# Kernel tuning notes

Measured on AMD Instinct MI355X. Metric: run time of the kernel, lower is better.

The kernel has to match this reference:

```python
import jax, jax.numpy as jnp
import numpy as np

N_NODES = 100000
N_EDGES = 3200000
F_IN = 128
HIDDEN = 16
F_OUT = 2


def setup_inputs() -> dict:
    key = jax.random.key(0)
    k1, k2, k3, k4 = jax.random.split(key, 4)
    x = jax.random.normal(k1, (N_NODES, F_IN), dtype=jnp.float32)
    edge_index = jax.random.randint(k2, (2, N_EDGES), 0, N_NODES, dtype=jnp.int64)
    # Glorot-ish init like torch_geometric's GCNConv linear layers
    W1 = jax.random.normal(k3, (F_IN, HIDDEN), dtype=jnp.float32) * (1.0 / np.sqrt(F_IN))
    b1 = jnp.zeros((HIDDEN,), dtype=jnp.float32)
    W2 = jax.random.normal(k4, (HIDDEN, F_OUT), dtype=jnp.float32) * (1.0 / np.sqrt(HIDDEN))
    b2 = jnp.zeros((F_OUT,), dtype=jnp.float32)
    return {"x": x, "edge_index": edge_index, "W1": W1, "b1": b1, "W2": W2, "b2": b2}


def _gcn_conv(x, src, dst, W, b, num_nodes):
    """PyG GCNConv: out = D^{-1/2}(A+I)D^{-1/2} X W + b (self-loops included in src/dst)."""
    h = x @ W  # [N, F_out]
    ones = jnp.ones(src.shape[0], dtype=h.dtype)
    deg = jax.ops.segment_sum(ones, dst, num_segments=num_nodes)  # in-degree incl. self-loop
    deg_inv_sqrt = jnp.where(deg > 0, jax.lax.rsqrt(jnp.maximum(deg, 1.0)), 0.0)
    norm = deg_inv_sqrt[src] * deg_inv_sqrt[dst]  # [E+N]
    msg = h[src] * norm[:, None]  # gather + scale: [E+N, F_out]
    out = jax.ops.segment_sum(msg, dst, num_segments=num_nodes)  # scatter-add
    return out + b


def reference(x, edge_index, W1, b1, W2, b2):
    num_nodes = x.shape[0]
    self_loops = jnp.arange(num_nodes, dtype=edge_index.dtype)
    src = jnp.concatenate([edge_index[0], self_loops])
    dst = jnp.concatenate([edge_index[1], self_loops])
    h = jax.nn.relu(_gcn_conv(x, src, dst, W1, b1, num_nodes))
    # F.dropout(training=self.training) is identity in eval mode
    out = _gcn_conv(h, src, dst, W2, b2, num_nodes)
    return out
```

## Files before the change

kernel.cpp:

```cpp
#include <hip/hip_runtime.h>

#define N_NODES 100000
#define N_EDGES 3200000
#define F_IN    128
#define HIDDEN  16
#define F_OUT   2

#define BSZ     256
#define NB      391
#define NPAD    (NB * BSZ)
#define G       800
#define EPB     (N_EDGES / G)
#define DUMMY_E 100000u

typedef float  f32x4 __attribute__((ext_vector_type(4)));
typedef float  f32x2 __attribute__((ext_vector_type(2)));
typedef _Float16 half8 __attribute__((ext_vector_type(8)));
typedef _Float16 half4 __attribute__((ext_vector_type(4)));

__global__ __launch_bounds__(256) void k_hist(const int* __restrict__ dst,
                                              unsigned* __restrict__ blockHist) {
    __shared__ unsigned h0[NB];
    __shared__ unsigned h1[NB];
    int t = threadIdx.x, g = blockIdx.x;
    for (int i = t; i < NB; i += 256) { h0[i] = 0u; h1[i] = 0u; }
    __syncthreads();
    const int2* d2 = (const int2*)(dst + g * EPB);
    unsigned* myh = (t & 1) ? h1 : h0;
    for (int i = t; i < EPB / 2; i += 256) {
        int2 v = d2[i];
        atomicAdd(&myh[(unsigned)v.x >> 8], 1u);
        atomicAdd(&myh[(unsigned)v.y >> 8], 1u);
    }
    __syncthreads();
    for (int i = t; i < NB; i += 256) blockHist[i * G + g] = h0[i] + h1[i];
}

__global__ __launch_bounds__(1024) void k_scan_blocks(unsigned* __restrict__ blockHist,
                                                      unsigned* __restrict__ total) {
    __shared__ unsigned s[1024];
    int b = blockIdx.x, t = threadIdx.x;
    unsigned v = (t < G) ? blockHist[b * G + t] : 0u;
    s[t] = v;
    __syncthreads();
    for (int off = 1; off < 1024; off <<= 1) {
        unsigned xv = (t >= off) ? s[t - off] : 0u;
        __syncthreads();
        s[t] += xv;
        __syncthreads();
    }
    if (t < G) blockHist[b * G + t] = s[t] - v;
    if (t == 1023) total[b] = s[t];
}

__global__ __launch_bounds__(512) void k_scan_buckets(const unsigned* __restrict__ total,
                                                      unsigned* __restrict__ bucketBase,
                                                      int* __restrict__ rowstart) {
    __shared__ unsigned s[512];
    int t = threadIdx.x;
    unsigned v = (t < NB) ? total[t] : 0u;
    s[t] = v;
    __syncthreads();
    for (int off = 1; off < 512; off <<= 1) {
        unsigned xv = (t >= off) ? s[t - off] : 0u;
        __syncthreads();
        s[t] += xv;
        __syncthreads();
    }
    if (t < NB) bucketBase[t] = s[t] - v;
    if (t == 511) {
        bucketBase[NB] = s[t];
        rowstart[N_NODES] = (int)s[t];
    }
}

__global__ __launch_bounds__(256) void k_scatter(const int* __restrict__ src,
                                                 const int* __restrict__ dst,
                                                 const unsigned* __restrict__ blockHist,
                                                 const unsigned* __restrict__ bucketBase,
                                                 unsigned* __restrict__ adj) {
    __shared__ unsigned stage[EPB];
    __shared__ unsigned short stage_b[EPB];
    __shared__ unsigned hist[NB];
    __shared__ unsigned h1[NB];
    __shared__ unsigned lstart[NB];
    __shared__ unsigned gbase[NB];
    __shared__ unsigned ssum[256];
    int t = threadIdx.x, g = blockIdx.x;
    for (int i = t; i < NB; i += 256) {
        hist[i] = 0u; h1[i] = 0u;
        gbase[i] = bucketBase[i] + blockHist[i * G + g];
    }
    __syncthreads();
    const int2* s2 = (const int2*)(src + g * EPB);
    const int2* d2 = (const int2*)(dst + g * EPB);
    unsigned* myh = (t & 1) ? h1 : hist;
    for (int i = t; i < EPB / 2; i += 256) {
        int2 v = d2[i];
        atomicAdd(&myh[(unsigned)v.x >> 8], 1u);
        atomicAdd(&myh[(unsigned)v.y >> 8], 1u);
    }
    __syncthreads();
    int i0 = t * 2;
    unsigned v0 = (i0 + 0 < NB) ? hist[i0 + 0] + h1[i0 + 0] : 0u;
    unsigned v1 = (i0 + 1 < NB) ? hist[i0 + 1] + h1[i0 + 1] : 0u;
    unsigned my = v0 + v1;
    ssum[t] = my;
    __syncthreads();
    for (int off = 1; off < 256; off <<= 1) {
        unsigned xv = (t >= off) ? ssum[t - off] : 0u;
        __syncthreads();
        ssum[t] += xv;
        __syncthreads();
    }
    unsigned e0 = ssum[t] - my;
    __syncthreads();
    unsigned e1 = e0 + v0;
    if (i0 + 0 < NB) { lstart[i0 + 0] = e0; hist[i0 + 0] = e0; }
    if (i0 + 1 < NB) { lstart[i0 + 1] = e1; hist[i0 + 1] = e1; }
    __syncthreads();
    for (int i = t; i < EPB / 2; i += 256) {
        int2 sv = s2[i], dv = d2[i];
        unsigned bkt0 = (unsigned)dv.x >> 8;
        unsigned pos0 = atomicAdd(&hist[bkt0], 1u);
        stage[pos0] = ((unsigned)(dv.x & 255) << 17) | (unsigned)sv.x;
        stage_b[pos0] = (unsigned short)bkt0;
        unsigned bkt1 = (unsigned)dv.y >> 8;
        unsigned pos1 = atomicAdd(&hist[bkt1], 1u);
        stage[pos1] = ((unsigned)(dv.y & 255) << 17) | (unsigned)sv.y;
        stage_b[pos1] = (unsigned short)bkt1;
    }
    __syncthreads();
    for (int j = t; j < EPB; j += 256) {
        unsigned bkt = stage_b[j];
        adj[gbase[bkt] + (j - lstart[bkt])] = stage[j];
    }
}

__global__ __launch_bounds__(512) void k_sortbucket(const unsigned* __restrict__ adj,
                                                    const unsigned* __restrict__ bucketBase,
                                                    unsigned* __restrict__ adj2,
                                                    int* __restrict__ rowstart,
                                                    float* __restrict__ dinv) {
    __shared__ unsigned hist[BSZ];
    __shared__ unsigned sc[BSZ];
    __shared__ unsigned cur[BSZ];
    int b = blockIdx.x, t = threadIdx.x;
    if (t < BSZ) hist[t] = 0u;
    __syncthreads();
    int e0 = (int)bucketBase[b], e1 = (int)bucketBase[b + 1];
    for (int i = e0 + t; i < e1; i += 512) atomicAdd(&hist[adj[i] >> 17], 1u);
    __syncthreads();
    if (t < BSZ) sc[t] = hist[t];
    __syncthreads();
    for (int off = 1; off < BSZ; off <<= 1) {
        unsigned a = 0;
        if (t < BSZ && t >= off) a = sc[t - off];
        __syncthreads();
        if (t < BSZ) sc[t] += a;
        __syncthreads();
    }
    if (t < BSZ) {
        unsigned excl = sc[t] - hist[t];
        cur[t] = (unsigned)e0 + excl;
        int node = b * BSZ + t;
        if (node < N_NODES) {
            rowstart[node] = e0 + (int)excl;
            dinv[node] = rsqrtf((float)(hist[t] + 1u));
        }
    }
    __syncthreads();
    for (int i = e0 + t; i < e1; i += 512) {
        unsigned v = adj[i];
        unsigned pos = atomicAdd(&cur[v >> 17], 1u);
        adj2[pos] = v & 0x1FFFFu;
    }
}

#define MM1_NODES 64
#define SXP 132
__global__ __launch_bounds__(256) void k_mm1(const float* __restrict__ x,
                                             const float* __restrict__ W1,
                                             const float* __restrict__ dinv,
                                             half4* __restrict__ hs) {
    __shared__ float sW[F_IN * HIDDEN];
    __shared__ float sX[MM1_NODES * SXP];
    int t = threadIdx.x;
    for (int i = t; i < F_IN * HIDDEN; i += 256) sW[i] = W1[i];
    int node0 = blockIdx.x * MM1_NODES;
    const float4* xv = (const float4*)(x + (size_t)node0 * F_IN);
    int maxv = (N_NODES - node0) * (F_IN / 4);
    if (maxv < 0) maxv = 0;
    for (int i = t; i < MM1_NODES * (F_IN / 4); i += 256) {
        if (i < maxv) {
            int nl = i >> 5, f4 = i & 31;
            ((float4*)(sX + nl * SXP))[f4] = xv[i];
        }
    }
    __syncthreads();
    int lane4 = t & 3;
    int nl = t >> 2;
    int n = node0 + nl;
    if (n >= NPAD) return;
    if (n >= N_NODES) {
        half4 hz = {(_Float16)0.f, (_Float16)0.f, (_Float16)0.f, (_Float16)0.f};
        hs[(size_t)n * 4 + lane4] = hz;
        return;
    }
    const float4* sWv = (const float4*)sW;
    float4 a = {0.f, 0.f, 0.f, 0.f};
    #pragma unroll 8
    for (int f = 0; f < F_IN; ++f) {
        float xval = sX[nl * SXP + f];
        float4 w = sWv[f * 4 + lane4];
        a.x = fmaf(xval, w.x, a.x);
        a.y = fmaf(xval, w.y, a.y);
        a.z = fmaf(xval, w.z, a.z);
        a.w = fmaf(xval, w.w, a.w);
    }
    float dv = dinv[n];
    half4 h; h[0] = (_Float16)(a.x * dv); h[1] = (_Float16)(a.y * dv);
    h[2] = (_Float16)(a.z * dv); h[3] = (_Float16)(a.w * dv);
    hs[(size_t)n * 4 + lane4] = h;
}

__global__ __launch_bounds__(256) void k_agg1(const unsigned* __restrict__ adj2,
                                              const int* __restrict__ rowstart,
                                              const char* __restrict__ hs,
                                              const float* __restrict__ dinv,
                                              const float* __restrict__ b1,
                                              const float* __restrict__ W2,
                                              float2* __restrict__ hs2) {
    int g = blockIdx.x * 256 + threadIdx.x;
    int node = g >> 1, le = g & 1;
    if (node >= N_NODES) {
        if (le == 0 && node < NPAD) { float2 z = {0.f, 0.f}; hs2[node] = z; }
        return;
    }
    int rs = rowstart[node], re = rowstart[node + 1];
    unsigned le16 = (unsigned)le * 16u;
    unsigned dummy_off = DUMMY_E * 32u + le16;

    float a0 = 0.f, a1 = 0.f, a2 = 0.f, a3 = 0.f, a4 = 0.f, a5 = 0.f, a6 = 0.f, a7 = 0.f;
    f32x4 w0, w1, w2, w3, w4, w5, w6, w7;

#define GL1(dst, o) asm volatile("global_load_dwordx4 %0, %1, %2" \
    : "=v"(dst) : "v"(o), "s"(hs) : "memory");
#define AC1(w_) { half8 h8; __builtin_memcpy(&h8, &w_, 16); \
    a0 += (float)h8[0]; a1 += (float)h8[1]; a2 += (float)h8[2]; a3 += (float)h8[3]; \
    a4 += (float)h8[4]; a5 += (float)h8[5]; a6 += (float)h8[6]; a7 += (float)h8[7]; }

    for (int bs = rs; bs < re; bs += 8) {
        const unsigned* ap = adj2 + bs;
        unsigned j0 = ap[0], j1 = ap[1], j2 = ap[2], j3 = ap[3];
        unsigned j4 = ap[4], j5 = ap[5], j6 = ap[6], j7 = ap[7];
        unsigned o0 = (bs + 0 < re) ? (j0 << 5) + le16 : dummy_off;
        unsigned o1 = (bs + 1 < re) ? (j1 << 5) + le16 : dummy_off;
        unsigned o2 = (bs + 2 < re) ? (j2 << 5) + le16 : dummy_off;
        unsigned o3 = (bs + 3 < re) ? (j3 << 5) + le16 : dummy_off;
        unsigned o4 = (bs + 4 < re) ? (j4 << 5) + le16 : dummy_off;
        unsigned o5 = (bs + 5 < re) ? (j5 << 5) + le16 : dummy_off;
        unsigned o6 = (bs + 6 < re) ? (j6 << 5) + le16 : dummy_off;
        unsigned o7 = (bs + 7 < re) ? (j7 << 5) + le16 : dummy_off;
        GL1(w0, o0) GL1(w1, o1) GL1(w2, o2) GL1(w3, o3)
        GL1(w4, o4) GL1(w5, o5) GL1(w6, o6) GL1(w7, o7)
        asm volatile("s_waitcnt vmcnt(0)" ::: "memory");
        __builtin_amdgcn_sched_barrier(0);
        AC1(w0) AC1(w1) AC1(w2) AC1(w3) AC1(w4) AC1(w5) AC1(w6) AC1(w7)
    }
    const _Float16* selfrow = (const _Float16*)(hs + (size_t)node * 32 + le16);
    float dv = dinv[node];
    float q0 = dv * (a0 + (float)selfrow[0]), q1 = dv * (a1 + (float)selfrow[1]);
    float q2 = dv * (a2 + (float)selfrow[2]), q3 = dv * (a3 + (float)selfrow[3]);
    float q4 = dv * (a4 + (float)selfrow[4]), q5 = dv * (a5 + (float)selfrow[5]);
    float q6 = dv * (a6 + (float)selfrow[6]), q7 = dv * (a7 + (float)selfrow[7]);
    const float4* b1v = (const float4*)(b1 + le * 8);
    float4 ba = b1v[0], bb = b1v[1];
    const float4* w2v = (const float4*)(W2 + le * 16);
    float4 wA = w2v[0], wB = w2v[1], wC = w2v[2], wD = w2v[3];
    float p0 = 0.f, p1 = 0.f, r;
    r = fmaxf(q0 + ba.x, 0.f); p0 = fmaf(r, wA.x, p0); p1 = fmaf(r, wA.y, p1);
    r = fmaxf(q1 + ba.y, 0.f); p0 = fmaf(r, wA.z, p0); p1 = fmaf(r, wA.w, p1);
    r = fmaxf(q2 + ba.z, 0.f); p0 = fmaf(r, wB.x, p0); p1 = fmaf(r, wB.y, p1);
    r = fmaxf(q3 + ba.w, 0.f); p0 = fmaf(r, wB.z, p0); p1 = fmaf(r, wB.w, p1);
    r = fmaxf(q4 + bb.x, 0.f); p0 = fmaf(r, wC.x, p0); p1 = fmaf(r, wC.y, p1);
    r = fmaxf(q5 + bb.y, 0.f); p0 = fmaf(r, wC.z, p0); p1 = fmaf(r, wC.w, p1);
    r = fmaxf(q6 + bb.z, 0.f); p0 = fmaf(r, wD.x, p0); p1 = fmaf(r, wD.y, p1);
    r = fmaxf(q7 + bb.w, 0.f); p0 = fmaf(r, wD.z, p0); p1 = fmaf(r, wD.w, p1);
    p0 += __shfl_xor(p0, 1);
    p1 += __shfl_xor(p1, 1);
    if (le == 0) {
        float2 h2; h2.x = p0 * dv; h2.y = p1 * dv;
        hs2[node] = h2;
    }
}

__global__ __launch_bounds__(256) void k_agg2(const unsigned* __restrict__ adj2,
                                              const int* __restrict__ rowstart,
                                              const char* __restrict__ hs2,
                                              const float* __restrict__ dinv,
                                              const float* __restrict__ b2,
                                              float2* __restrict__ out) {
    int node = blockIdx.x * 256 + threadIdx.x;
    if (node >= N_NODES) return;
    int rs = rowstart[node], re = rowstart[node + 1];
    unsigned dummy_off = DUMMY_E * 8u;

    float a0 = 0.f, a1 = 0.f;
    f32x2 w0, w1, w2, w3, w4, w5, w6, w7;

#define GL2(dst, o) asm volatile("global_load_dwordx2 %0, %1, %2" \
    : "=v"(dst) : "v"(o), "s"(hs2) : "memory");

    for (int bs = rs; bs < re; bs += 8) {
        const unsigned* ap = adj2 + bs;
        unsigned j0 = ap[0], j1 = ap[1], j2 = ap[2], j3 = ap[3];
        unsigned j4 = ap[4], j5 = ap[5], j6 = ap[6], j7 = ap[7];
        unsigned o0 = (bs + 0 < re) ? (j0 << 3) : dummy_off;
        unsigned o1 = (bs + 1 < re) ? (j1 << 3) : dummy_off;
        unsigned o2 = (bs + 2 < re) ? (j2 << 3) : dummy_off;
        unsigned o3 = (bs + 3 < re) ? (j3 << 3) : dummy_off;
        unsigned o4 = (bs + 4 < re) ? (j4 << 3) : dummy_off;
        unsigned o5 = (bs + 5 < re) ? (j5 << 3) : dummy_off;
        unsigned o6 = (bs + 6 < re) ? (j6 << 3) : dummy_off;
        unsigned o7 = (bs + 7 < re) ? (j7 << 3) : dummy_off;
        GL2(w0, o0) GL2(w1, o1) GL2(w2, o2) GL2(w3, o3)
        GL2(w4, o4) GL2(w5, o5) GL2(w6, o6) GL2(w7, o7)
        asm volatile("s_waitcnt vmcnt(0)" ::: "memory");
        __builtin_amdgcn_sched_barrier(0);
        a0 += w0[0] + w1[0] + w2[0] + w3[0] + w4[0] + w5[0] + w6[0] + w7[0];
        a1 += w0[1] + w1[1] + w2[1] + w3[1] + w4[1] + w5[1] + w6[1] + w7[1];
    }
    const float2* h2p = (const float2*)hs2;
    float2 selfv = h2p[node];
    float dv = dinv[node];
    float2 r;
    r.x = fmaf(dv, a0 + selfv.x, b2[0]);
    r.y = fmaf(dv, a1 + selfv.y, b2[1]);
    out[node] = r;
}

extern "C" void kernel_launch(void* const* d_in, const int* in_sizes, int n_in,
                              void* d_out, int out_size, void* d_ws, size_t ws_size,
                              hipStream_t stream) {
    const float* x   = (const float*)d_in[0];
    const int*   ei  = (const int*)d_in[1];
    const int*   srcv = ei;
    const int*   dstv = ei + N_EDGES;
    const float* W1  = (const float*)d_in[2];
    const float* b1  = (const float*)d_in[3];
    const float* W2  = (const float*)d_in[4];
    const float* b2  = (const float*)d_in[5];
    float* out = (float*)d_out;

    char* w = (char*)d_ws;
    unsigned* adj        = (unsigned*)w;  w += (size_t)N_EDGES * 4;
    unsigned* adj2       = (unsigned*)w;  w += (size_t)(N_EDGES + 8) * 4;
    unsigned* blockHist  = (unsigned*)w;  w += (size_t)NB * G * 4;
    unsigned* total      = (unsigned*)w;  w += (size_t)NB * 4;
    unsigned* bucketBase = (unsigned*)w;  w += (size_t)(NB + 1) * 4;
    int*      rowstart   = (int*)w;       w += (size_t)(N_NODES + 1) * 4;
    w = (char*)(((size_t)w + 15) & ~(size_t)15);
    float* dinv  = (float*)w;  w += (size_t)N_NODES * 4;
    char*  hs    = w;          w += (size_t)NPAD * HIDDEN * 2;
    float* hs2   = (float*)w;

    k_hist        <<<G, 256, 0, stream>>>(dstv, blockHist);
    k_scan_blocks <<<NB, 1024, 0, stream>>>(blockHist, total);
    k_scan_buckets<<<1, 512, 0, stream>>>(total, bucketBase, rowstart);
    k_scatter     <<<G, 256, 0, stream>>>(srcv, dstv, blockHist, bucketBase, adj);
    k_sortbucket  <<<NB, 512, 0, stream>>>(adj, bucketBase, adj2, rowstart, dinv);
    k_mm1         <<<NPAD / MM1_NODES, 256, 0, stream>>>(x, W1, dinv, (half4*)hs);
    k_agg1        <<<(2 * NPAD) / 256, 256, 0, stream>>>(adj2, rowstart, hs, dinv,
                                                         b1, W2, (float2*)hs2);
    k_agg2        <<<(NPAD + 255) / 256, 256, 0, stream>>>(adj2, rowstart, (const char*)hs2,
                                                           dinv, b2, (float2*)out);
}
```

Measured before the change: 125.0 us.

## Fuse bucket scan into block scan and fold first matmul into bucket sort

Merges the two scan kernels using a last-block ticket counter, so the final bucket-level scan runs in whichever block finishes last instead of a separate single-block launch. Folds the X·W1 transform into the per-bucket sort kernel, reusing the in-shared degree/dinv and reading x rows directly, with two threads per node combined by a lane shuffle. This removes two kernel launches and a dinv round trip through global memory. In exchange, the sort kernel now needs more shared memory for W1 and does the matmul with only 391 blocks, which may reduce parallelism for that phase.

```diff
diff --git a/kernel.cpp b/kernel.cpp
--- a/kernel.cpp
+++ b/kernel.cpp
@@ -19,10 +19,12 @@
 typedef _Float16 half4 __attribute__((ext_vector_type(4)));
 
 __global__ __launch_bounds__(256) void k_hist(const int* __restrict__ dst,
-                                              unsigned* __restrict__ blockHist) {
+                                              unsigned* __restrict__ blockHist,
+                                              unsigned* __restrict__ done) {
     __shared__ unsigned h0[NB];
     __shared__ unsigned h1[NB];
     int t = threadIdx.x, g = blockIdx.x;
+    if (g == 0 && t == 0) *done = 0u;
     for (int i = t; i < NB; i += 256) { h0[i] = 0u; h1[i] = 0u; }
     __syncthreads();
     const int2* d2 = (const int2*)(dst + g * EPB);
@@ -36,9 +38,13 @@
     for (int i = t; i < NB; i += 256) blockHist[i * G + g] = h0[i] + h1[i];
 }
 
-__global__ __launch_bounds__(1024) void k_scan_blocks(unsigned* __restrict__ blockHist,
-                                                      unsigned* __restrict__ total) {
+__global__ __launch_bounds__(1024) void k_scan(unsigned* __restrict__ blockHist,
+                                               unsigned* __restrict__ total,
+                                               unsigned* __restrict__ bucketBase,
+                                               int* __restrict__ rowstart,
+                                               unsigned* __restrict__ done) {
     __shared__ unsigned s[1024];
+    __shared__ unsigned ticket_s;
     int b = blockIdx.x, t = threadIdx.x;
     unsigned v = (t < G) ? blockHist[b * G + t] : 0u;
     s[t] = v;
@@ -51,26 +57,26 @@
     }
     if (t < G) blockHist[b * G + t] = s[t] - v;
     if (t == 1023) total[b] = s[t];
-}
-
-__global__ __launch_bounds__(512) void k_scan_buckets(const unsigned* __restrict__ total,
-                                                      unsigned* __restrict__ bucketBase,
-                                                      int* __restrict__ rowstart) {
-    __shared__ unsigned s[512];
-    int t = threadIdx.x;
-    unsigned v = (t < NB) ? total[t] : 0u;
-    s[t] = v;
-    __syncthreads();
-    for (int off = 1; off < 512; off <<= 1) {
-        unsigned xv = (t >= off) ? s[t - off] : 0u;
-        __syncthreads();
-        s[t] += xv;
-        __syncthreads();
-    }
-    if (t < NB) bucketBase[t] = s[t] - v;
-    if (t == 511) {
-        bucketBase[NB] = s[t];
-        rowstart[N_NODES] = (int)s[t];
+    __threadfence();
+    __syncthreads();
+    if (t == 0) ticket_s = atomicAdd(done, 1u);
+    __syncthreads();
+    if (ticket_s == NB - 1) {
+        __threadfence();
+        unsigned w0 = (t < NB) ? total[t] : 0u;
+        s[t] = w0;
+        __syncthreads();
+        for (int off = 1; off < 1024; off <<= 1) {
+            unsigned xv = (t >= off) ? s[t - off] : 0u;
+            __syncthreads();
+            s[t] += xv;
+            __syncthreads();
+        }
+        if (t < NB) bucketBase[t] = s[t] - w0;
+        if (t == 1023) {
+            bucketBase[NB] = s[t];
+            rowstart[N_NODES] = (int)s[t];
+        }
     }
 }
 
@@ -137,15 +143,21 @@
     }
 }
 
-__global__ __launch_bounds__(512) void k_sortbucket(const unsigned* __restrict__ adj,
-                                                    const unsigned* __restrict__ bucketBase,
-                                                    unsigned* __restrict__ adj2,
-                                                    int* __restrict__ rowstart,
-                                                    float* __restrict__ dinv) {
+__global__ __launch_bounds__(512) void k_sortmm(const unsigned* __restrict__ adj,
+                                                const unsigned* __restrict__ bucketBase,
+                                                const float* __restrict__ x,
+                                                const float* __restrict__ W1,
+                                                unsigned* __restrict__ adj2,
+                                                int* __restrict__ rowstart,
+                                                float* __restrict__ dinv,
+                                                char* __restrict__ hs) {
+    __shared__ float sW[F_IN * HIDDEN];
     __shared__ unsigned hist[BSZ];
     __shared__ unsigned sc[BSZ];
     __shared__ unsigned cur[BSZ];
+    __shared__ float sdinv[BSZ];
     int b = blockIdx.x, t = threadIdx.x;
+    for (int i = t; i < F_IN * HIDDEN; i += 512) sW[i] = W1[i];
     if (t < BSZ) hist[t] = 0u;
     __syncthreads();
     int e0 = (int)bucketBase[b], e1 = (int)bucketBase[b + 1];
@@ -161,12 +173,15 @@
         __syncthreads();
     }
     if (t < BSZ) {
-        unsigned excl = sc[t] - hist[t];
+        unsigned deg = hist[t];
+        unsigned excl = sc[t] - deg;
         cur[t] = (unsigned)e0 + excl;
+        float dv = rsqrtf((float)(deg + 1u));
+        sdinv[t] = dv;
         int node = b * BSZ + t;
         if (node < N_NODES) {
             rowstart[node] = e0 + (int)excl;
-            dinv[node] = rsqrtf((float)(hist[t] + 1u));
+            dinv[node] = dv;
         }
     }
     __syncthreads();
@@ -175,53 +190,48 @@
         unsigned pos = atomicAdd(&cur[v >> 17], 1u);
         adj2[pos] = v & 0x1FFFFu;
     }
-}
-
-#define MM1_NODES 64
-#define SXP 132
-__global__ __launch_bounds__(256) void k_mm1(const float* __restrict__ x,
-                                             const float* __restrict__ W1,
-                                             const float* __restrict__ dinv,
-                                             half4* __restrict__ hs) {
-    __shared__ float sW[F_IN * HIDDEN];
-    __shared__ float sX[MM1_NODES * SXP];
-    int t = threadIdx.x;
-    for (int i = t; i < F_IN * HIDDEN; i += 256) sW[i] = W1[i];
-    int node0 = blockIdx.x * MM1_NODES;
-    const float4* xv = (const float4*)(x + (size_t)node0 * F_IN);
-    int maxv = (N_NODES - node0) * (F_IN / 4);
-    if (maxv < 0) maxv = 0;
-    for (int i = t; i < MM1_NODES * (F_IN / 4); i += 256) {
-        if (i < maxv) {
-            int nl = i >> 5, f4 = i & 31;
-            ((float4*)(sX + nl * SXP))[f4] = xv[i];
+    int nl = t >> 1, half = t & 1;
+    int node = b * BSZ + nl;
+    if (node >= N_NODES) {
+        half8 hz = {(_Float16)0.f, (_Float16)0.f, (_Float16)0.f, (_Float16)0.f,
+                    (_Float16)0.f, (_Float16)0.f, (_Float16)0.f, (_Float16)0.f};
+        if (node < NPAD) *(half8*)(hs + (size_t)node * 32 + half * 16) = hz;
+        return;
+    }
+    const f32x4* xr = (const f32x4*)(x + (size_t)node * F_IN + half * 64);
+    const f32x4* wv = (const f32x4*)sW;
+    f32x4 a0 = {0.f,0.f,0.f,0.f}, a1 = a0, a2 = a0, a3 = a0;
+    #pragma unroll 4
+    for (int k = 0; k < 16; ++k) {
+        f32x4 xq = xr[k];
+        int f0 = (half << 6) + (k << 2);
+        #pragma unroll
+        for (int j = 0; j < 4; ++j) {
+            float xv = xq[j];
+            const f32x4* wr = wv + (size_t)(f0 + j) * 4;
+            a0 += xv * wr[0];
+            a1 += xv * wr[1];
+            a2 += xv * wr[2];
+            a3 += xv * wr[3];
         }
     }
-    __syncthreads();
-    int lane4 = t & 3;
-    int nl = t >> 2;
-    int n = node0 + nl;
-    if (n >= NPAD) return;
-    if (n >= N_NODES) {
-        half4 hz = {(_Float16)0.f, (_Float16)0.f, (_Float16)0.f, (_Float16)0.f};
-        hs[(size_t)n * 4 + lane4] = hz;
-        return;
-    }
-    const float4* sWv = (const float4*)sW;
-    float4 a = {0.f, 0.f, 0.f, 0.f};
-    #pragma unroll 8
-    for (int f = 0; f < F_IN; ++f) {
-        float xval = sX[nl * SXP + f];
-        float4 w = sWv[f * 4 + lane4];
-        a.x = fmaf(xval, w.x, a.x);
-        a.y = fmaf(xval, w.y, a.y);
-        a.z = fmaf(xval, w.z, a.z);
-        a.w = fmaf(xval, w.w, a.w);
-    }
-    float dv = dinv[n];
-    half4 h; h[0] = (_Float16)(a.x * dv); h[1] = (_Float16)(a.y * dv);
-    h[2] = (_Float16)(a.z * dv); h[3] = (_Float16)(a.w * dv);
-    hs[(size_t)n * 4 + lane4] = h;
+    a0[0] += __shfl_xor(a0[0], 1); a0[1] += __shfl_xor(a0[1], 1);
+    a0[2] += __shfl_xor(a0[2], 1); a0[3] += __shfl_xor(a0[3], 1);
+    a1[0] += __shfl_xor(a1[0], 1); a1[1] += __shfl_xor(a1[1], 1);
+    a1[2] += __shfl_xor(a1[2], 1); a1[3] += __shfl_xor(a1[3], 1);
+    a2[0] += __shfl_xor(a2[0], 1); a2[1] += __shfl_xor(a2[1], 1);
+    a2[2] += __shfl_xor(a2[2], 1); a2[3] += __shfl_xor(a2[3], 1);
+    a3[0] += __shfl_xor(a3[0], 1); a3[1] += __shfl_xor(a3[1], 1);
+    a3[2] += __shfl_xor(a3[2], 1); a3[3] += __shfl_xor(a3[3], 1);
+    float dv = sdinv[nl];
+    f32x4 u = half ? a2 : a0;
+    f32x4 v2 = half ? a3 : a1;
+    half8 hh;
+    hh[0] = (_Float16)(u[0] * dv);  hh[1] = (_Float16)(u[1] * dv);
+    hh[2] = (_Float16)(u[2] * dv);  hh[3] = (_Float16)(u[3] * dv);
+    hh[4] = (_Float16)(v2[0] * dv); hh[5] = (_Float16)(v2[1] * dv);
+    hh[6] = (_Float16)(v2[2] * dv); hh[7] = (_Float16)(v2[3] * dv);
+    *(half8*)(hs + (size_t)node * 32 + half * 16) = hh;
 }
 
 __global__ __launch_bounds__(256) void k_agg1(const unsigned* __restrict__ adj2,
@@ -359,20 +369,19 @@
     unsigned* blockHist  = (unsigned*)w;  w += (size_t)NB * G * 4;
     unsigned* total      = (unsigned*)w;  w += (size_t)NB * 4;
     unsigned* bucketBase = (unsigned*)w;  w += (size_t)(NB + 1) * 4;
+    unsigned* done       = (unsigned*)w;  w += 16;
     int*      rowstart   = (int*)w;       w += (size_t)(N_NODES + 1) * 4;
     w = (char*)(((size_t)w + 15) & ~(size_t)15);
     float* dinv  = (float*)w;  w += (size_t)N_NODES * 4;
     char*  hs    = w;          w += (size_t)NPAD * HIDDEN * 2;
     float* hs2   = (float*)w;
 
-    k_hist        <<<G, 256, 0, stream>>>(dstv, blockHist);
-    k_scan_blocks <<<NB, 1024, 0, stream>>>(blockHist, total);
-    k_scan_buckets<<<1, 512, 0, stream>>>(total, bucketBase, rowstart);
-    k_scatter     <<<G, 256, 0, stream>>>(srcv, dstv, blockHist, bucketBase, adj);
-    k_sortbucket  <<<NB, 512, 0, stream>>>(adj, bucketBase, adj2, rowstart, dinv);
-    k_mm1         <<<NPAD / MM1_NODES, 256, 0, stream>>>(x, W1, dinv, (half4*)hs);
-    k_agg1        <<<(2 * NPAD) / 256, 256, 0, stream>>>(adj2, rowstart, hs, dinv,
-                                                         b1, W2, (float2*)hs2);
-    k_agg2        <<<(NPAD + 255) / 256, 256, 0, stream>>>(adj2, rowstart, (const char*)hs2,
-                                                           dinv, b2, (float2*)out);
-}
+    k_hist    <<<G, 256, 0, stream>>>(dstv, blockHist, done);
+    k_scan    <<<NB, 1024, 0, stream>>>(blockHist, total, bucketBase, rowstart, done);
+    k_scatter <<<G, 256, 0, stream>>>(srcv, dstv, blockHist, bucketBase, adj);
+    k_sortmm  <<<NB, 512, 0, stream>>>(adj, bucketBase, x, W1, adj2, rowstart, dinv, hs);
+    k_agg1    <<<(2 * NPAD) / 256, 256, 0, stream>>>(adj2, rowstart, hs, dinv,
+                                                     b1, W2, (float2*)hs2);
+    k_agg2    <<<(NPAD + 255) / 256, 256, 0, stream>>>(adj2, rowstart, (const char*)hs2,
+                                                       dinv, b2, (float2*)out);
+}
```

Result: slower. 229.1 us (+83.3%).

## Fuse first-layer matmul into bucket sort kernel and widen scatter blocks

Applied to the files above, without the earlier changes.

Merges the X·W1 projection into the per-bucket sort kernel, so each 256-node bucket block also computes the scaled half-precision hidden features using its shared-memory dinv. This removes one launch and the global dinv reload. It also doubles the thread count of the histogram and scatter kernels to 512, which simplifies the local scan to one bucket per thread. The trade-off is that the fused kernel runs only 391 blocks with more shared memory each, so the matmul gets less parallelism than the old separate launch.

```diff
diff --git a/kernel.cpp b/kernel.cpp
--- a/kernel.cpp
+++ b/kernel.cpp
@@ -16,24 +16,24 @@
 typedef float  f32x4 __attribute__((ext_vector_type(4)));
 typedef float  f32x2 __attribute__((ext_vector_type(2)));
 typedef _Float16 half8 __attribute__((ext_vector_type(8)));
-typedef _Float16 half4 __attribute__((ext_vector_type(4)));
-
-__global__ __launch_bounds__(256) void k_hist(const int* __restrict__ dst,
+typedef _Float16 half2v __attribute__((ext_vector_type(2)));
+
+__global__ __launch_bounds__(512) void k_hist(const int* __restrict__ dst,
                                               unsigned* __restrict__ blockHist) {
     __shared__ unsigned h0[NB];
     __shared__ unsigned h1[NB];
     int t = threadIdx.x, g = blockIdx.x;
-    for (int i = t; i < NB; i += 256) { h0[i] = 0u; h1[i] = 0u; }
+    for (int i = t; i < NB; i += 512) { h0[i] = 0u; h1[i] = 0u; }
     __syncthreads();
     const int2* d2 = (const int2*)(dst + g * EPB);
     unsigned* myh = (t & 1) ? h1 : h0;
-    for (int i = t; i < EPB / 2; i += 256) {
+    for (int i = t; i < EPB / 2; i += 512) {
         int2 v = d2[i];
         atomicAdd(&myh[(unsigned)v.x >> 8], 1u);
         atomicAdd(&myh[(unsigned)v.y >> 8], 1u);
     }
     __syncthreads();
-    for (int i = t; i < NB; i += 256) blockHist[i * G + g] = h0[i] + h1[i];
+    for (int i = t; i < NB; i += 512) blockHist[i * G + g] = h0[i] + h1[i];
 }
 
 __global__ __launch_bounds__(1024) void k_scan_blocks(unsigned* __restrict__ blockHist,
@@ -74,7 +74,7 @@
     }
 }
 
-__global__ __launch_bounds__(256) void k_scatter(const int* __restrict__ src,
+__global__ __launch_bounds__(512) void k_scatter(const int* __restrict__ src,
                                                  const int* __restrict__ dst,
                                                  const unsigned* __restrict__ blockHist,
                                                  const unsigned* __restrict__ bucketBase,
@@ -85,9 +85,9 @@
     __shared__ unsigned h1[NB];
     __shared__ unsigned lstart[NB];
     __shared__ unsigned gbase[NB];
-    __shared__ unsigned ssum[256];
+    __shared__ unsigned ssum[512];
     int t = threadIdx.x, g = blockIdx.x;
-    for (int i = t; i < NB; i += 256) {
+    for (int i = t; i < NB; i += 512) {
         hist[i] = 0u; h1[i] = 0u;
         gbase[i] = bucketBase[i] + blockHist[i * G + g];
     }
@@ -95,31 +95,25 @@
     const int2* s2 = (const int2*)(src + g * EPB);
     const int2* d2 = (const int2*)(dst + g * EPB);
     unsigned* myh = (t & 1) ? h1 : hist;
-    for (int i = t; i < EPB / 2; i += 256) {
+    for (int i = t; i < EPB / 2; i += 512) {
         int2 v = d2[i];
         atomicAdd(&myh[(unsigned)v.x >> 8], 1u);
         atomicAdd(&myh[(unsigned)v.y >> 8], 1u);
     }
     __syncthreads();
-    int i0 = t * 2;
-    unsigned v0 = (i0 + 0 < NB) ? hist[i0 + 0] + h1[i0 + 0] : 0u;
-    unsigned v1 = (i0 + 1 < NB) ? hist[i0 + 1] + h1[i0 + 1] : 0u;
-    unsigned my = v0 + v1;
-    ssum[t] = my;
-    __syncthreads();
-    for (int off = 1; off < 256; off <<= 1) {
+    unsigned v0 = (t < NB) ? hist[t] + h1[t] : 0u;
+    ssum[t] = v0;
+    __syncthreads();
+    for (int off = 1; off < 512; off <<= 1) {
         unsigned xv = (t >= off) ? ssum[t - off] : 0u;
         __syncthreads();
         ssum[t] += xv;
         __syncthreads();
     }
-    unsigned e0 = ssum[t] - my;
-    __syncthreads();
-    unsigned e1 = e0 + v0;
-    if (i0 + 0 < NB) { lstart[i0 + 0] = e0; hist[i0 + 0] = e0; }
-    if (i0 + 1 < NB) { lstart[i0 + 1] = e1; hist[i0 + 1] = e1; }
-    __syncthreads();
-    for (int i = t; i < EPB / 2; i += 256) {
+    unsigned e0 = ssum[t] - v0;
+    if (t < NB) { lstart[t] = e0; hist[t] = e0; }
+    __syncthreads();
+    for (int i = t; i < EPB / 2; i += 512) {
         int2 sv = s2[i], dv = d2[i];
         unsigned bkt0 = (unsigned)dv.x >> 8;
         unsigned pos0 = atomicAdd(&hist[bkt0], 1u);
@@ -131,21 +125,29 @@
         stage_b[pos1] = (unsigned short)bkt1;
     }
     __syncthreads();
-    for (int j = t; j < EPB; j += 256) {
+    for (int j = t; j < EPB; j += 512) {
         unsigned bkt = stage_b[j];
         adj[gbase[bkt] + (j - lstart[bkt])] = stage[j];
     }
 }
 
-__global__ __launch_bounds__(512) void k_sortbucket(const unsigned* __restrict__ adj,
-                                                    const unsigned* __restrict__ bucketBase,
-                                                    unsigned* __restrict__ adj2,
-                                                    int* __restrict__ rowstart,
-                                                    float* __restrict__ dinv) {
+#define SXP 132
+__global__ __launch_bounds__(512) void k_sortmm(const unsigned* __restrict__ adj,
+                                                const unsigned* __restrict__ bucketBase,
+                                                const float* __restrict__ x,
+                                                const float* __restrict__ W1,
+                                                unsigned* __restrict__ adj2,
+                                                int* __restrict__ rowstart,
+                                                float* __restrict__ dinv,
+                                                char* __restrict__ hs) {
+    __shared__ float sW[F_IN * HIDDEN];
+    __shared__ float sX[64 * SXP];
     __shared__ unsigned hist[BSZ];
     __shared__ unsigned sc[BSZ];
     __shared__ unsigned cur[BSZ];
+    __shared__ float sdinv[BSZ];
     int b = blockIdx.x, t = threadIdx.x;
+    for (int i = t; i < F_IN * HIDDEN; i += 512) sW[i] = W1[i];
     if (t < BSZ) hist[t] = 0u;
     __syncthreads();
     int e0 = (int)bucketBase[b], e1 = (int)bucketBase[b + 1];
@@ -161,12 +163,15 @@
         __syncthreads();
     }
     if (t < BSZ) {
-        unsigned excl = sc[t] - hist[t];
+        unsigned deg = hist[t];
+        unsigned excl = sc[t] - deg;
         cur[t] = (unsigned)e0 + excl;
+        float dv = rsqrtf((float)(deg + 1u));
+        sdinv[t] = dv;
         int node = b * BSZ + t;
         if (node < N_NODES) {
             rowstart[node] = e0 + (int)excl;
-            dinv[node] = rsqrtf((float)(hist[t] + 1u));
+            dinv[node] = dv;
         }
     }
     __syncthreads();
@@ -175,53 +180,39 @@
         unsigned pos = atomicAdd(&cur[v >> 17], 1u);
         adj2[pos] = v & 0x1FFFFu;
     }
-}
-
-#define MM1_NODES 64
-#define SXP 132
-__global__ __launch_bounds__(256) void k_mm1(const float* __restrict__ x,
-                                             const float* __restrict__ W1,
-                                             const float* __restrict__ dinv,
-                                             half4* __restrict__ hs) {
-    __shared__ float sW[F_IN * HIDDEN];
-    __shared__ float sX[MM1_NODES * SXP];
-    int t = threadIdx.x;
-    for (int i = t; i < F_IN * HIDDEN; i += 256) sW[i] = W1[i];
-    int node0 = blockIdx.x * MM1_NODES;
-    const float4* xv = (const float4*)(x + (size_t)node0 * F_IN);
-    int maxv = (N_NODES - node0) * (F_IN / 4);
-    if (maxv < 0) maxv = 0;
-    for (int i = t; i < MM1_NODES * (F_IN / 4); i += 256) {
-        if (i < maxv) {
-            int nl = i >> 5, f4 = i & 31;
-            ((float4*)(sX + nl * SXP))[f4] = xv[i];
+    int nl = t >> 3;
+    int c8 = t & 7;
+    for (int tile = 0; tile < 4; ++tile) {
+        int node0 = b * BSZ + tile * 64;
+        __syncthreads();
+        const float4* xv = (const float4*)(x + (size_t)node0 * F_IN);
+        int maxv = (N_NODES - node0) * (F_IN / 4);
+        if (maxv < 0) maxv = 0;
+        for (int i = t; i < 64 * (F_IN / 4); i += 512) {
+            if (i < maxv) {
+                int nn = i >> 5, f4 = i & 31;
+                ((float4*)(sX + nn * SXP))[f4] = xv[i];
+            }
         }
-    }
-    __syncthreads();
-    int lane4 = t & 3;
-    int nl = t >> 2;
-    int n = node0 + nl;
-    if (n >= NPAD) return;
-    if (n >= N_NODES) {
-        half4 hz = {(_Float16)0.f, (_Float16)0.f, (_Float16)0.f, (_Float16)0.f};
-        hs[(size_t)n * 4 + lane4] = hz;
-        return;
-    }
-    const float4* sWv = (const float4*)sW;
-    float4 a = {0.f, 0.f, 0.f, 0.f};
-    #pragma unroll 8
-    for (int f = 0; f < F_IN; ++f) {
-        float xval = sX[nl * SXP + f];
-        float4 w = sWv[f * 4 + lane4];
-        a.x = fmaf(xval, w.x, a.x);
-        a.y = fmaf(xval, w.y, a.y);
-        a.z = fmaf(xval, w.z, a.z);
-        a.w = fmaf(xval, w.w, a.w);
-    }
-    float dv = dinv[n];
-    half4 h; h[0] = (_Float16)(a.x * dv); h[1] = (_Float16)(a.y * dv);
-    h[2] = (_Float16)(a.z * dv); h[3] = (_Float16)(a.w * dv);
-    hs[(size_t)n * 4 + lane4] = h;
+        __syncthreads();
+        int node = node0 + nl;
+        float acc0 = 0.f, acc1 = 0.f;
+        const f32x2* sW2 = (const f32x2*)sW;
+        #pragma unroll 8
+        for (int f = 0; f < F_IN; ++f) {
+            float xval = sX[nl * SXP + f];
+            f32x2 wv = sW2[f * 8 + c8];
+            acc0 = fmaf(xval, wv[0], acc0);
+            acc1 = fmaf(xval, wv[1], acc1);
+        }
+        if (node < NPAD) {
+            float dv = (node < N_NODES) ? sdinv[tile * 64 + nl] : 0.f;
+            half2v h2;
+            h2[0] = (_Float16)(acc0 * dv);
+            h2[1] = (_Float16)(acc1 * dv);
+            *(half2v*)(hs + (size_t)node * 32 + c8 * 4) = h2;
+        }
+    }
 }
 
 __global__ __launch_bounds__(256) void k_agg1(const unsigned* __restrict__ adj2,
@@ -365,12 +356,11 @@
     char*  hs    = w;          w += (size_t)NPAD * HIDDEN * 2;
     float* hs2   = (float*)w;
 
-    k_hist        <<<G, 256, 0, stream>>>(dstv, blockHist);
+    k_hist        <<<G, 512, 0, stream>>>(dstv, blockHist);
     k_scan_blocks <<<NB, 1024, 0, stream>>>(blockHist, total);
     k_scan_buckets<<<1, 512, 0, stream>>>(total, bucketBase, rowstart);
-    k_scatter     <<<G, 256, 0, stream>>>(srcv, dstv, blockHist, bucketBase, adj);
-    k_sortbucket  <<<NB, 512, 0, stream>>>(adj, bucketBase, adj2, rowstart, dinv);
-    k_mm1         <<<NPAD / MM1_NODES, 256, 0, stream>>>(x, W1, dinv, (half4*)hs);
+    k_scatter     <<<G, 512, 0, stream>>>(srcv, dstv, blockHist, bucketBase, adj);
+    k_sortmm      <<<NB, 512, 0, stream>>>(adj, bucketBase, x, W1, adj2, rowstart, dinv, hs);
     k_agg1        <<<(2 * NPAD) / 256, 256, 0, stream>>>(adj2, rowstart, hs, dinv,
                                                          b1, W2, (float2*)hs2);
     k_agg2        <<<(NPAD + 255) / 256, 256, 0, stream>>>(adj2, rowstart, (const char*)hs2,
```

Measured after the change: 129.0 us. 1.03x slower.
